# Kernel tuning notes

Hardware: AMD Instinct MI355X
Metric: run time of the kernel (lower is better)

The kernel has to match this reference:

```python
import jax, jax.numpy as jnp
import numpy as np

B, H, W, D, N, C = 32, 64, 64, 512, 512, 512  # batch, feat-map H/W, dim_attention, n, channels


def setup_inputs() -> dict:
    key = jax.random.key(0)
    k0, k1, k2, k3, k4 = jax.random.split(key, 5)
    ctx_val = jax.random.normal(k0, (B, C, H, W), jnp.float32)
    ctx_key = jax.random.normal(k1, (B, H, W, D), jnp.float32)
    ctx_mask = jnp.ones((B, H, W), jnp.float32)
    ht_query = jax.random.normal(k2, (B, N), jnp.float32)
    # fc_query: Linear(n -> dim_attention, bias=False); weight [D, N]
    Wq = jax.random.normal(k3, (D, N), jnp.float32) * (1.0 / np.sqrt(N))
    # fc_attention: Linear(dim_attention -> 1); weight [1, D], bias [1]
    Wa = jax.random.normal(k4, (1, D), jnp.float32) * (1.0 / np.sqrt(D))
    ba = jnp.zeros((1,), jnp.float32)
    return {"ctx_val": ctx_val, "ctx_key": ctx_key, "ctx_mask": ctx_mask,
            "ht_query": ht_query, "Wq": Wq, "Wa": Wa, "ba": ba}


def reference(ctx_val, ctx_key, ctx_mask, ht_query, Wq, Wa, ba):
    # project query: [B, N] @ [N, D] -> [B, D]
    q = ht_query @ Wq.T
    # additive attention score: tanh(key + q) -> scalar per location
    e = jnp.tanh(ctx_key + q[:, None, None, :])          # [B, H, W, D]
    s = jnp.einsum("bhwd,d->bhw", e, Wa[0]) + ba[0]        # [B, H, W]
    # global max-subtract (as in original: attention_score.max() over all elems)
    s = jnp.exp(s - jnp.max(s)) * ctx_mask                 # [B, H, W]
    s = s / (jnp.sum(s, axis=(1, 2), keepdims=True) + 1e-10)
    # weighted context: sum over H, W
    ct = jnp.einsum("bchw,bhw->bc", ctx_val, s)            # [B, C]
    return ct, s
```

## Files before the change

### kernel.cpp

```cpp
#include <hip/hip_runtime.h>
#include <math.h>

#define BB   32
#define DD   512
#define NN   512
#define CC   512
#define HW   4096
#define NLOC (BB * HW)
#define NBD  (BB * DD)
#define NBC  (BB * CC)

__device__ __forceinline__ float wave_reduce_sum(float v) {
#pragma unroll
    for (int m = 1; m < 64; m <<= 1) v += __shfl_xor(v, m, 64);
    return v;
}

__device__ __forceinline__ float wave_reduce_max(float v) {
#pragma unroll
    for (int m = 1; m < 64; m <<= 1) v = fmaxf(v, __shfl_xor(v, m, 64));
    return v;
}

__device__ __forceinline__ float tanh_fast(float x) {
    float t = __expf(2.0f * x);
    return 1.0f - 2.0f * __builtin_amdgcn_rcpf(t + 1.0f);
}

__global__ void qproj_kernel(const float* __restrict__ hq,
                             const float* __restrict__ Wq,
                             float* __restrict__ q) {
    int wid  = threadIdx.x >> 6;
    int lane = threadIdx.x & 63;
    int idx  = blockIdx.x * 4 + wid;
    int b = idx >> 9;
    int d = idx & 511;
    const float* hrow = hq + (size_t)b * NN;
    const float* wrow = Wq + (size_t)d * NN;
    float acc = 0.0f;
#pragma unroll
    for (int j = 0; j < 2; ++j) {
        int n = j * 256 + lane * 4;
        float4 h = *(const float4*)(hrow + n);
        float4 w = *(const float4*)(wrow + n);
        acc += h.x * w.x + h.y * w.y + h.z * w.z + h.w * w.w;
    }
    acc = wave_reduce_sum(acc);
    if (lane == 0) q[idx] = acc;
}

__global__ void score_kernel(const float* __restrict__ key,
                             const float* __restrict__ q,
                             const float* __restrict__ Wa,
                             const float* __restrict__ ba,
                             float* __restrict__ s_raw,
                             float* __restrict__ blkmax) {
    __shared__ float smax[4];
    int wid  = threadIdx.x >> 6;
    int lane = threadIdx.x & 63;
    int idx  = blockIdx.x * 4 + wid;
    int b = idx >> 12;
    const float* krow = key + (size_t)idx * DD;
    const float* qrow = q + (size_t)b * DD;
    float acc = 0.0f;
#pragma unroll
    for (int j = 0; j < 2; ++j) {
        int n = j * 256 + lane * 4;
        float4 k = *(const float4*)(krow + n);
        float4 qq = *(const float4*)(qrow + n);
        float4 w = *(const float4*)(Wa + n);
        acc += w.x * tanh_fast(k.x + qq.x);
        acc += w.y * tanh_fast(k.y + qq.y);
        acc += w.z * tanh_fast(k.z + qq.z);
        acc += w.w * tanh_fast(k.w + qq.w);
    }
    acc = wave_reduce_sum(acc);
    float s = acc + ba[0];
    if (lane == 0) { s_raw[idx] = s; smax[wid] = s; }
    __syncthreads();
    if (threadIdx.x == 0) {
        blkmax[blockIdx.x] = fmaxf(fmaxf(smax[0], smax[1]), fmaxf(smax[2], smax[3]));
    }
}

__global__ void maxred_kernel(const float* __restrict__ blkmax, int n,
                              float* __restrict__ gmax) {
    __shared__ float sm[16];
    float m = -INFINITY;
    for (int i = threadIdx.x; i < n; i += 1024) m = fmaxf(m, blkmax[i]);
    m = wave_reduce_max(m);
    int wid = threadIdx.x >> 6, lane = threadIdx.x & 63;
    if (lane == 0) sm[wid] = m;
    __syncthreads();
    if (threadIdx.x == 0) {
        float g = sm[0];
#pragma unroll
        for (int i = 1; i < 16; ++i) g = fmaxf(g, sm[i]);
        gmax[0] = g;
    }
}

__global__ void softmax_kernel(const float* __restrict__ s_raw,
                               const float* __restrict__ mask,
                               const float* __restrict__ gmax,
                               float* __restrict__ s_out) {
    __shared__ float sm[4];
    int b = blockIdx.x;
    float gm = gmax[0];
    size_t base = (size_t)b * HW;
    float e[16];
    float psum = 0.0f;
#pragma unroll
    for (int j = 0; j < 16; ++j) {
        int i = j * 256 + threadIdx.x;
        float v = __expf(s_raw[base + i] - gm) * mask[base + i];
        e[j] = v;
        psum += v;
    }
    psum = wave_reduce_sum(psum);
    int wid = threadIdx.x >> 6, lane = threadIdx.x & 63;
    if (lane == 0) sm[wid] = psum;
    __syncthreads();
    float total = sm[0] + sm[1] + sm[2] + sm[3];
    float inv = 1.0f / (total + 1e-10f);
#pragma unroll
    for (int j = 0; j < 16; ++j) {
        int i = j * 256 + threadIdx.x;
        s_out[base + i] = e[j] * inv;
    }
}

__global__ void ct_kernel(const float* __restrict__ val,
                          const float* __restrict__ s,
                          float* __restrict__ ct) {
    int wid  = threadIdx.x >> 6;
    int lane = threadIdx.x & 63;
    int idx  = blockIdx.x * 4 + wid;
    int b = idx >> 9;
    const float* vrow = val + (size_t)idx * HW;
    const float* srow = s + (size_t)b * HW;
    float acc = 0.0f;
#pragma unroll
    for (int j = 0; j < 16; ++j) {
        int h = j * 256 + lane * 4;
        float4 v = *(const float4*)(vrow + h);
        float4 w = *(const float4*)(srow + h);
        acc += v.x * w.x + v.y * w.y + v.z * w.z + v.w * w.w;
    }
    acc = wave_reduce_sum(acc);
    if (lane == 0) ct[idx] = acc;
}

extern "C" void kernel_launch(void* const* d_in, const int* in_sizes, int n_in,
                              void* d_out, int out_size, void* d_ws, size_t ws_size,
                              hipStream_t stream) {
    const float* ctx_val  = (const float*)d_in[0];
    const float* ctx_key  = (const float*)d_in[1];
    const float* ctx_mask = (const float*)d_in[2];
    const float* ht_query = (const float*)d_in[3];
    const float* Wq       = (const float*)d_in[4];
    const float* Wa       = (const float*)d_in[5];
    const float* ba       = (const float*)d_in[6];

    float* ct_out = (float*)d_out;
    float* s_out  = (float*)d_out + NBC;

    float* ws     = (float*)d_ws;
    float* q      = ws;
    float* s_raw  = ws + NBD;
    float* blkmax = ws + NBD + NLOC;
    float* gmax   = ws + NBD + NLOC + NLOC / 4;

    const int SCORE_BLOCKS = NLOC / 4;

    qproj_kernel<<<NBD / 4, 256, 0, stream>>>(ht_query, Wq, q);
    score_kernel<<<SCORE_BLOCKS, 256, 0, stream>>>(ctx_key, q, Wa, ba, s_raw, blkmax);
    maxred_kernel<<<1, 1024, 0, stream>>>(blkmax, SCORE_BLOCKS, gmax);
    softmax_kernel<<<BB, 256, 0, stream>>>(s_raw, ctx_mask, gmax, s_out);
    ct_kernel<<<NBC / 4, 256, 0, stream>>>(ctx_val, s_out, ct_out);
}
```

Before: 510.3 us.

## Drop global max pass, fuse exp into score kernel, defer normalization into ct

The global max subtraction is removed. Scores are exponentiated directly in the score kernel, with per-wave partial sums, which eliminates the max-reduction kernel and the raw score buffer. The ct kernel reads unnormalized exponentials and applies the per-batch inverse denominator at the end, and each wave handles two channel rows to reuse the weight loads. This is mathematically equivalent, but it risks overflow if the scores grow large, because the max shift is no longer applied. The query projection also reuses the loaded query row across four outputs per wave.

```diff
diff --git a/kernel.cpp b/kernel.cpp
--- a/kernel.cpp
+++ b/kernel.cpp
@@ -10,16 +10,17 @@
 #define NBD  (BB * DD)
 #define NBC  (BB * CC)
 
+#define SCORE_WAVES 8192
+#define LPW (NLOC / SCORE_WAVES)
+
 __device__ __forceinline__ float wave_reduce_sum(float v) {
 #pragma unroll
     for (int m = 1; m < 64; m <<= 1) v += __shfl_xor(v, m, 64);
     return v;
 }
 
-__device__ __forceinline__ float wave_reduce_max(float v) {
-#pragma unroll
-    for (int m = 1; m < 64; m <<= 1) v = fmaxf(v, __shfl_xor(v, m, 64));
-    return v;
+__device__ __forceinline__ float dot4(float4 a, float4 b) {
+    return a.x * b.x + a.y * b.y + a.z * b.z + a.w * b.w;
 }
 
 __device__ __forceinline__ float tanh_fast(float x) {
@@ -32,123 +33,127 @@
                              float* __restrict__ q) {
     int wid  = threadIdx.x >> 6;
     int lane = threadIdx.x & 63;
-    int idx  = blockIdx.x * 4 + wid;
-    int b = idx >> 9;
-    int d = idx & 511;
+    int wave = blockIdx.x * 4 + wid;
+    int base = wave * 4;
+    int b = base >> 9;
     const float* hrow = hq + (size_t)b * NN;
-    const float* wrow = Wq + (size_t)d * NN;
-    float acc = 0.0f;
+    float4 h0 = *(const float4*)(hrow + lane * 8);
+    float4 h1 = *(const float4*)(hrow + lane * 8 + 4);
 #pragma unroll
-    for (int j = 0; j < 2; ++j) {
-        int n = j * 256 + lane * 4;
-        float4 h = *(const float4*)(hrow + n);
-        float4 w = *(const float4*)(wrow + n);
-        acc += h.x * w.x + h.y * w.y + h.z * w.z + h.w * w.w;
-    }
-    acc = wave_reduce_sum(acc);
-    if (lane == 0) q[idx] = acc;
-}
-
-__global__ void score_kernel(const float* __restrict__ key,
-                             const float* __restrict__ q,
-                             const float* __restrict__ Wa,
-                             const float* __restrict__ ba,
-                             float* __restrict__ s_raw,
-                             float* __restrict__ blkmax) {
-    __shared__ float smax[4];
-    int wid  = threadIdx.x >> 6;
-    int lane = threadIdx.x & 63;
-    int idx  = blockIdx.x * 4 + wid;
-    int b = idx >> 12;
-    const float* krow = key + (size_t)idx * DD;
-    const float* qrow = q + (size_t)b * DD;
-    float acc = 0.0f;
-#pragma unroll
-    for (int j = 0; j < 2; ++j) {
-        int n = j * 256 + lane * 4;
-        float4 k = *(const float4*)(krow + n);
-        float4 qq = *(const float4*)(qrow + n);
-        float4 w = *(const float4*)(Wa + n);
-        acc += w.x * tanh_fast(k.x + qq.x);
-        acc += w.y * tanh_fast(k.y + qq.y);
-        acc += w.z * tanh_fast(k.z + qq.z);
-        acc += w.w * tanh_fast(k.w + qq.w);
-    }
-    acc = wave_reduce_sum(acc);
-    float s = acc + ba[0];
-    if (lane == 0) { s_raw[idx] = s; smax[wid] = s; }
-    __syncthreads();
-    if (threadIdx.x == 0) {
-        blkmax[blockIdx.x] = fmaxf(fmaxf(smax[0], smax[1]), fmaxf(smax[2], smax[3]));
+    for (int o = 0; o < 4; ++o) {
+        int idx = base + o;
+        int d = idx & 511;
+        const float* wrow = Wq + (size_t)d * NN;
+        float4 w0 = *(const float4*)(wrow + lane * 8);
+        float4 w1 = *(const float4*)(wrow + lane * 8 + 4);
+        float acc = dot4(h0, w0) + dot4(h1, w1);
+        acc = wave_reduce_sum(acc);
+        if (lane == 0) q[idx] = acc;
     }
 }
 
-__global__ void maxred_kernel(const float* __restrict__ blkmax, int n,
-                              float* __restrict__ gmax) {
-    __shared__ float sm[16];
-    float m = -INFINITY;
-    for (int i = threadIdx.x; i < n; i += 1024) m = fmaxf(m, blkmax[i]);
-    m = wave_reduce_max(m);
-    int wid = threadIdx.x >> 6, lane = threadIdx.x & 63;
-    if (lane == 0) sm[wid] = m;
-    __syncthreads();
-    if (threadIdx.x == 0) {
-        float g = sm[0];
-#pragma unroll
-        for (int i = 1; i < 16; ++i) g = fmaxf(g, sm[i]);
-        gmax[0] = g;
+__global__ void score_exp_kernel(const float* __restrict__ key,
+                                 const float* __restrict__ q,
+                                 const float* __restrict__ Wa,
+                                 const float* __restrict__ ba,
+                                 const float* __restrict__ mask,
+                                 float* __restrict__ ebuf,
+                                 float* __restrict__ partials) {
+    int wid  = threadIdx.x >> 6;
+    int lane = threadIdx.x & 63;
+    int gw   = blockIdx.x * 4 + wid;
+    int loc0 = gw * LPW;
+    int b    = loc0 >> 12;
+    const float* qrow = q + (size_t)b * DD;
+    float4 q0 = *(const float4*)(qrow + lane * 8);
+    float4 q1 = *(const float4*)(qrow + lane * 8 + 4);
+    float4 w0 = *(const float4*)(Wa + lane * 8);
+    float4 w1 = *(const float4*)(Wa + lane * 8 + 4);
+    float ba0 = ba[0];
+    float part = 0.0f;
+#pragma unroll 4
+    for (int t = 0; t < LPW; ++t) {
+        int loc = loc0 + t;
+        const float* krow = key + (size_t)loc * DD;
+        float4 k0 = *(const float4*)(krow + lane * 8);
+        float4 k1 = *(const float4*)(krow + lane * 8 + 4);
+        float acc;
+        acc  = w0.x * tanh_fast(k0.x + q0.x);
+        acc += w0.y * tanh_fast(k0.y + q0.y);
+        acc += w0.z * tanh_fast(k0.z + q0.z);
+        acc += w0.w * tanh_fast(k0.w + q0.w);
+        acc += w1.x * tanh_fast(k1.x + q1.x);
+        acc += w1.y * tanh_fast(k1.y + q1.y);
+        acc += w1.z * tanh_fast(k1.z + q1.z);
+        acc += w1.w * tanh_fast(k1.w + q1.w);
+        acc = wave_reduce_sum(acc);
+        if (lane == 0) {
+            float e = __expf(acc + ba0) * mask[loc];
+            ebuf[loc] = e;
+            part += e;
+        }
     }
+    if (lane == 0) partials[gw] = part;
 }
 
-__global__ void softmax_kernel(const float* __restrict__ s_raw,
-                               const float* __restrict__ mask,
-                               const float* __restrict__ gmax,
-                               float* __restrict__ s_out) {
+__global__ void denom_scale_kernel(const float* __restrict__ partials,
+                                   const float* __restrict__ ebuf,
+                                   float* __restrict__ inv_denom,
+                                   float* __restrict__ s_out) {
     __shared__ float sm[4];
     int b = blockIdx.x;
-    float gm = gmax[0];
-    size_t base = (size_t)b * HW;
-    float e[16];
-    float psum = 0.0f;
-#pragma unroll
-    for (int j = 0; j < 16; ++j) {
-        int i = j * 256 + threadIdx.x;
-        float v = __expf(s_raw[base + i] - gm) * mask[base + i];
-        e[j] = v;
-        psum += v;
-    }
-    psum = wave_reduce_sum(psum);
     int wid = threadIdx.x >> 6, lane = threadIdx.x & 63;
-    if (lane == 0) sm[wid] = psum;
+    float p = partials[b * 256 + threadIdx.x];
+    p = wave_reduce_sum(p);
+    if (lane == 0) sm[wid] = p;
     __syncthreads();
     float total = sm[0] + sm[1] + sm[2] + sm[3];
     float inv = 1.0f / (total + 1e-10f);
+    if (threadIdx.x == 0) inv_denom[b] = inv;
+    const float* erow = ebuf + (size_t)b * HW;
+    float* srow = s_out + (size_t)b * HW;
 #pragma unroll
-    for (int j = 0; j < 16; ++j) {
-        int i = j * 256 + threadIdx.x;
-        s_out[base + i] = e[j] * inv;
+    for (int t = 0; t < 4; ++t) {
+        int i = t * 1024 + threadIdx.x * 4;
+        float4 e = *(const float4*)(erow + i);
+        float4 r;
+        r.x = e.x * inv; r.y = e.y * inv; r.z = e.z * inv; r.w = e.w * inv;
+        *(float4*)(srow + i) = r;
     }
 }
 
 __global__ void ct_kernel(const float* __restrict__ val,
-                          const float* __restrict__ s,
+                          const float* __restrict__ ebuf,
+                          const float* __restrict__ inv_denom,
                           float* __restrict__ ct) {
     int wid  = threadIdx.x >> 6;
     int lane = threadIdx.x & 63;
-    int idx  = blockIdx.x * 4 + wid;
-    int b = idx >> 9;
-    const float* vrow = val + (size_t)idx * HW;
-    const float* srow = s + (size_t)b * HW;
-    float acc = 0.0f;
-#pragma unroll
-    for (int j = 0; j < 16; ++j) {
-        int h = j * 256 + lane * 4;
-        float4 v = *(const float4*)(vrow + h);
-        float4 w = *(const float4*)(srow + h);
-        acc += v.x * w.x + v.y * w.y + v.z * w.z + v.w * w.w;
+    int gw   = blockIdx.x * 4 + wid;
+    int idx0 = gw * 2;
+    int b = idx0 >> 9;
+    float inv = inv_denom[b];
+    const float* erow = ebuf + (size_t)b * HW;
+    const float* v0 = val + (size_t)idx0 * HW;
+    const float* v1 = v0 + HW;
+    float acc0 = 0.0f, acc1 = 0.0f;
+#pragma unroll 4
+    for (int t = 0; t < 8; ++t) {
+        int h = t * 512 + lane * 8;
+        float4 e0 = *(const float4*)(erow + h);
+        float4 e1 = *(const float4*)(erow + h + 4);
+        float4 a0 = *(const float4*)(v0 + h);
+        float4 a1 = *(const float4*)(v0 + h + 4);
+        float4 c0 = *(const float4*)(v1 + h);
+        float4 c1 = *(const float4*)(v1 + h + 4);
+        acc0 += dot4(a0, e0) + dot4(a1, e1);
+        acc1 += dot4(c0, e0) + dot4(c1, e1);
     }
-    acc = wave_reduce_sum(acc);
-    if (lane == 0) ct[idx] = acc;
+    acc0 = wave_reduce_sum(acc0);
+    acc1 = wave_reduce_sum(acc1);
+    if (lane == 0) {
+        ct[idx0]     = acc0 * inv;
+        ct[idx0 + 1] = acc1 * inv;
+    }
 }
 
 extern "C" void kernel_launch(void* const* d_in, const int* in_sizes, int n_in,
@@ -165,17 +170,15 @@
     float* ct_out = (float*)d_out;
     float* s_out  = (float*)d_out + NBC;
 
-    float* ws     = (float*)d_ws;
-    float* q      = ws;
-    float* s_raw  = ws + NBD;
-    float* blkmax = ws + NBD + NLOC;
-    float* gmax   = ws + NBD + NLOC + NLOC / 4;
+    float* ws       = (float*)d_ws;
+    float* q        = ws;
+    float* ebuf     = ws + NBD;
+    float* partials = ws + NBD + NLOC;
+    float* invd     = ws + NBD + NLOC + SCORE_WAVES;
 
-    const int SCORE_BLOCKS = NLOC / 4;
-
-    qproj_kernel<<<NBD / 4, 256, 0, stream>>>(ht_query, Wq, q);
-    score_kernel<<<SCORE_BLOCKS, 256, 0, stream>>>(ctx_key, q, Wa, ba, s_raw, blkmax);
-    maxred_kernel<<<1, 1024, 0, stream>>>(blkmax, SCORE_BLOCKS, gmax);
-    softmax_kernel<<<BB, 256, 0, stream>>>(s_raw, ctx_mask, gmax, s_out);
-    ct_kernel<<<NBC / 4, 256, 0, stream>>>(ctx_val, s_out, ct_out);
+    qproj_kernel<<<1024, 256, 0, stream>>>(ht_query, Wq, q);
+    score_exp_kernel<<<2048, 256, 0, stream>>>(ctx_key, q, Wa, ba, ctx_mask,
+                                               ebuf, partials);
+    denom_scale_kernel<<<BB, 256, 0, stream>>>(partials, ebuf, invd, s_out);
+    ct_kernel<<<2048, 256, 0, stream>>>(ctx_val, ebuf, invd, ct_out);
 }
```

After: 522.4 us. 1.02x slower.
